# Optimization experiments

Measured on AMD Instinct MI355X. Metric: run time of the kernel, lower is better.

## Reference

```python
import jax, jax.numpy as jnp
import numpy as np


def _procrustes_align(X, Y):
    """Batched similarity-transform (scipy-style Procrustes, reflection allowed).
    Aligns Y (pred) to X (target). X, Y: [B, N, 3]. Returns aligned Y: [B, N, 3].
    """
    muX = X.mean(axis=1, keepdims=True)                      # [B,1,3]
    muY = Y.mean(axis=1, keepdims=True)
    X0 = X - muX
    Y0 = Y - muY
    normX = jnp.sqrt((X0 ** 2).sum(axis=(1, 2), keepdims=True))  # [B,1,1]
    normY = jnp.sqrt((Y0 ** 2).sum(axis=(1, 2), keepdims=True))
    X0n = X0 / normX
    Y0n = Y0 / normY
    # 3x3 cross-covariance per batch element
    M = jnp.einsum('bni,bnj->bij', X0n, Y0n)                 # [B,3,3]
    U, s, Vt = jnp.linalg.svd(M)                             # batched tiny SVD
    # Optimal rotation Q = V @ U^T = (U @ Vt)^T  (minimizes ||Y0n @ Q - X0n||)
    Q = jnp.swapaxes(jnp.matmul(U, Vt), -1, -2)              # [B,3,3]
    traceTA = s.sum(-1)[:, None, None]                       # [B,1,1]
    Z = normX * traceTA * jnp.einsum('bni,bij->bnj', Y0n, Q) + muX
    return Z


def setup_inputs() -> dict:
    key = jax.random.key(0)
    k1, k2 = jax.random.split(key)
    B, N = 262144, 21
    pred_kp3d = jax.random.normal(k1, (B, N, 3), dtype=jnp.float32)
    target_kp3d = jax.random.normal(k2, (B, N, 3), dtype=jnp.float32)
    return {"pred_kp3d": pred_kp3d, "target_kp3d": target_kp3d}


def reference(pred_kp3d, target_kp3d):
    pred_aligned = _procrustes_align(target_kp3d, pred_kp3d)
    # mean per-joint Euclidean distance (PA-MPJPE style)
    err = jnp.sqrt(((pred_aligned - target_kp3d) ** 2).sum(-1)).mean()
    return err
```

## Files before the change

### kernel.cpp

```cpp
#include <hip/hip_runtime.h>
#include <math.h>

#define NPTS 21
#define FLB  63
#define BPB  128
#define THREADS 128
#define NVEC (BPB * FLB / 4)
#define FULL_ROUNDS (NVEC / THREADS)
#define TAIL_LANES  (NVEC % THREADS)

__device__ __forceinline__ void async_cp16(const float* g, float* l) {
    __builtin_amdgcn_global_load_lds(
        (__attribute__((address_space(1))) void*)g,
        (__attribute__((address_space(3))) void*)l,
        16, 0, 0);
}

__global__ __launch_bounds__(THREADS)
void pa_mpjpe(const float* __restrict__ pred,
              const float* __restrict__ targ,
              float* __restrict__ ws,
              int B)
{
    __shared__ __align__(16) float sbuf[BPB * FLB];
    __shared__ float swsum[THREADS / 64];

    const int tid  = threadIdx.x;
    const int lane_u = tid & ~63;
    const int b0   = blockIdx.x * BPB;

    {
        const float* gp = pred + (size_t)b0 * FLB;
        #pragma unroll
        for (int j = 0; j < FULL_ROUNDS; ++j)
            async_cp16(gp + 4 * (j * THREADS + tid), sbuf + 4 * (j * THREADS + lane_u));
        if (tid < TAIL_LANES)
            async_cp16(gp + 4 * (FULL_ROUNDS * THREADS + tid),
                       sbuf + 4 * (FULL_ROUNDS * THREADS + lane_u));
    }
    __builtin_amdgcn_s_waitcnt(0x0F70);
    __syncthreads();

    float y[NPTS][3];
    float sy0 = 0.f, sy1 = 0.f, sy2 = 0.f, syy = 0.f;
    const int base = tid * FLB;
    #pragma unroll
    for (int n = 0; n < NPTS; ++n) {
        float a = sbuf[base + 3*n + 0];
        float b = sbuf[base + 3*n + 1];
        float c = sbuf[base + 3*n + 2];
        y[n][0] = a; y[n][1] = b; y[n][2] = c;
        sy0 += a; sy1 += b; sy2 += c;
        syy = fmaf(a, a, fmaf(b, b, fmaf(c, c, syy)));
    }
    __syncthreads();

    {
        const float* gt = targ + (size_t)b0 * FLB;
        #pragma unroll
        for (int j = 0; j < FULL_ROUNDS; ++j)
            async_cp16(gt + 4 * (j * THREADS + tid), sbuf + 4 * (j * THREADS + lane_u));
        if (tid < TAIL_LANES)
            async_cp16(gt + 4 * (FULL_ROUNDS * THREADS + tid),
                       sbuf + 4 * (FULL_ROUNDS * THREADS + lane_u));
    }
    __builtin_amdgcn_s_waitcnt(0x0F70);
    __syncthreads();

    float sx0 = 0.f, sx1 = 0.f, sx2 = 0.f;
    float m00=0,m01=0,m02=0, m10=0,m11=0,m12=0, m20=0,m21=0,m22=0;
    #pragma unroll
    for (int n = 0; n < NPTS; ++n) {
        float a = sbuf[base + 3*n + 0];
        float b = sbuf[base + 3*n + 1];
        float c = sbuf[base + 3*n + 2];
        sx0 += a; sx1 += b; sx2 += c;
        float u = y[n][0], v = y[n][1], w = y[n][2];
        m00 = fmaf(a,u,m00); m01 = fmaf(a,v,m01); m02 = fmaf(a,w,m02);
        m10 = fmaf(b,u,m10); m11 = fmaf(b,v,m11); m12 = fmaf(b,w,m12);
        m20 = fmaf(c,u,m20); m21 = fmaf(c,v,m21); m22 = fmaf(c,w,m22);
    }

    const float invN = 1.0f / (float)NPTS;
    float mux0 = sx0*invN, mux1 = sx1*invN, mux2 = sx2*invN;
    float muy0 = sy0*invN, muy1 = sy1*invN, muy2 = sy2*invN;
    float ny2  = syy - (sy0*sy0 + sy1*sy1 + sy2*sy2) * invN;
    float c00 = m00 - sx0*sy0*invN, c01 = m01 - sx0*sy1*invN, c02 = m02 - sx0*sy2*invN;
    float c10 = m10 - sx1*sy0*invN, c11 = m11 - sx1*sy1*invN, c12 = m12 - sx1*sy2*invN;
    float c20 = m20 - sx2*sy0*invN, c21 = m21 - sx2*sy1*invN, c22 = m22 - sx2*sy2*invN;

    float q00=c00, q01=c10, q02=c20,
          q10=c01, q11=c11, q12=c21,
          q20=c02, q21=c12, q22=c22;
    #pragma unroll
    for (int it = 0; it < 8; ++it) {
        float C00 = q11*q22 - q12*q21;
        float C01 = q12*q20 - q10*q22;
        float C02 = q10*q21 - q11*q20;
        float C10 = q02*q21 - q01*q22;
        float C11 = q00*q22 - q02*q20;
        float C12 = q01*q20 - q00*q21;
        float C20 = q01*q12 - q02*q11;
        float C21 = q02*q10 - q00*q12;
        float C22 = q00*q11 - q01*q10;
        float det = q00*C00 + q01*C01 + q02*C02;
        float ad  = fmaxf(fabsf(det), 1e-30f);
        float sdet = copysignf(ad, det);
        float g  = __expf(0.333333333f * __logf(ad));
        float ha = 0.5f / g;
        float hb = 0.5f * g / sdet;
        q00 = ha*q00 + hb*C00; q01 = ha*q01 + hb*C01; q02 = ha*q02 + hb*C02;
        q10 = ha*q10 + hb*C10; q11 = ha*q11 + hb*C11; q12 = ha*q12 + hb*C12;
        q20 = ha*q20 + hb*C20; q21 = ha*q21 + hb*C21; q22 = ha*q22 + hb*C22;
    }

    float trP = q00*c00 + q01*c10 + q02*c20
              + q10*c01 + q11*c11 + q12*c21
              + q20*c02 + q21*c12 + q22*c22;
    float k = trP / ny2;
    float r00=k*q00, r01=k*q01, r02=k*q02;
    float r10=k*q10, r11=k*q11, r12=k*q12;
    float r20=k*q20, r21=k*q21, r22=k*q22;

    float errsum = 0.0f;
    #pragma unroll
    for (int n = 0; n < NPTS; ++n) {
        float xa = sbuf[base + 3*n + 0];
        float xb = sbuf[base + 3*n + 1];
        float xc = sbuf[base + 3*n + 2];
        float u = y[n][0] - muy0, v = y[n][1] - muy1, w = y[n][2] - muy2;
        float z0 = fmaf(u, r00, fmaf(v, r10, fmaf(w, r20, mux0))) - xa;
        float z1 = fmaf(u, r01, fmaf(v, r11, fmaf(w, r21, mux1))) - xb;
        float z2 = fmaf(u, r02, fmaf(v, r12, fmaf(w, r22, mux2))) - xc;
        errsum += sqrtf(fmaf(z0, z0, fmaf(z1, z1, z2*z2)));
    }

    #pragma unroll
    for (int off = 32; off > 0; off >>= 1) errsum += __shfl_down(errsum, off, 64);
    if ((tid & 63) == 0) swsum[tid >> 6] = errsum;
    __syncthreads();
    if (tid == 0) ws[blockIdx.x] = swsum[0] + swsum[1];
}

__global__ __launch_bounds__(256)
void pa_reduce(const float* __restrict__ ws, float* __restrict__ out,
               int nblk, float inv_total)
{
    __shared__ float sw[4];
    float s = 0.0f;
    for (int i = threadIdx.x; i < nblk; i += 256) s += ws[i];
    #pragma unroll
    for (int off = 32; off > 0; off >>= 1) s += __shfl_down(s, off, 64);
    if ((threadIdx.x & 63) == 0) sw[threadIdx.x >> 6] = s;
    __syncthreads();
    if (threadIdx.x == 0)
        out[0] = (sw[0] + sw[1] + sw[2] + sw[3]) * inv_total;
}

extern "C" void kernel_launch(void* const* d_in, const int* in_sizes, int n_in,
                              void* d_out, int out_size, void* d_ws, size_t ws_size,
                              hipStream_t stream)
{
    const float* pred = (const float*)d_in[0];
    const float* targ = (const float*)d_in[1];
    float* out = (float*)d_out;
    float* ws  = (float*)d_ws;

    int B = in_sizes[0] / FLB;
    int grid = (B + BPB - 1) / BPB;
    float inv_total = 1.0f / ((float)B * (float)NPTS);

    pa_mpjpe<<<grid, THREADS, 0, stream>>>(pred, targ, ws, B);
    pa_reduce<<<1, 256, 0, stream>>>(ws, out, grid, inv_total);
}
```

Baseline: 149.8 us.

## Split each batch element across four lanes with shuffle reductions, smaller blocks

```diff
diff --git a/kernel.cpp b/kernel.cpp
--- a/kernel.cpp
+++ b/kernel.cpp
@@ -3,11 +3,11 @@
 
 #define NPTS 21
 #define FLB  63
-#define BPB  128
-#define THREADS 128
-#define NVEC (BPB * FLB / 4)
-#define FULL_ROUNDS (NVEC / THREADS)
-#define TAIL_LANES  (NVEC % THREADS)
+#define BPB  16
+#define THREADS 64
+#define TVEC (BPB * FLB / 4)
+#define FULLR (TVEC / THREADS)
+#define TAILL (TVEC % THREADS)
 
 __device__ __forceinline__ void async_cp16(const float* g, float* l) {
     __builtin_amdgcn_global_load_lds(
@@ -16,70 +16,67 @@
         16, 0, 0);
 }
 
-__global__ __launch_bounds__(THREADS)
+__global__ __launch_bounds__(THREADS, 5)
 void pa_mpjpe(const float* __restrict__ pred,
               const float* __restrict__ targ,
               float* __restrict__ ws,
               int B)
 {
-    __shared__ __align__(16) float sbuf[BPB * FLB];
-    __shared__ float swsum[THREADS / 64];
+    __shared__ __align__(16) float ly[BPB * FLB];
+    __shared__ __align__(16) float lx[BPB * FLB];
 
-    const int tid  = threadIdx.x;
-    const int lane_u = tid & ~63;
-    const int b0   = blockIdx.x * BPB;
+    const int tid = threadIdx.x;
+    const int b   = tid & (BPB - 1);
+    const int sub = tid >> 4;
+    const int b0  = blockIdx.x * BPB;
 
     {
         const float* gp = pred + (size_t)b0 * FLB;
+        const float* gt = targ + (size_t)b0 * FLB;
         #pragma unroll
-        for (int j = 0; j < FULL_ROUNDS; ++j)
-            async_cp16(gp + 4 * (j * THREADS + tid), sbuf + 4 * (j * THREADS + lane_u));
-        if (tid < TAIL_LANES)
-            async_cp16(gp + 4 * (FULL_ROUNDS * THREADS + tid),
-                       sbuf + 4 * (FULL_ROUNDS * THREADS + lane_u));
+        for (int j = 0; j < FULLR; ++j)
+            async_cp16(gp + 4 * (j * THREADS + tid), ly + 4 * (j * THREADS));
+        if (tid < TAILL)
+            async_cp16(gp + 4 * (FULLR * THREADS + tid), ly + 4 * (FULLR * THREADS));
+        #pragma unroll
+        for (int j = 0; j < FULLR; ++j)
+            async_cp16(gt + 4 * (j * THREADS + tid), lx + 4 * (j * THREADS));
+        if (tid < TAILL)
+            async_cp16(gt + 4 * (FULLR * THREADS + tid), lx + 4 * (FULLR * THREADS));
     }
     __builtin_amdgcn_s_waitcnt(0x0F70);
-    __syncthreads();
 
-    float y[NPTS][3];
-    float sy0 = 0.f, sy1 = 0.f, sy2 = 0.f, syy = 0.f;
-    const int base = tid * FLB;
+    float py0[6], py1[6], py2[6];
+    float sy0=0.f, sy1=0.f, sy2=0.f, syy=0.f;
+    float sx0=0.f, sx1=0.f, sx2=0.f;
+    float m00=0,m01=0,m02=0, m10=0,m11=0,m12=0, m20=0,m21=0,m22=0;
+    const int base = b * FLB;
     #pragma unroll
-    for (int n = 0; n < NPTS; ++n) {
-        float a = sbuf[base + 3*n + 0];
-        float b = sbuf[base + 3*n + 1];
-        float c = sbuf[base + 3*n + 2];
-        y[n][0] = a; y[n][1] = b; y[n][2] = c;
-        sy0 += a; sy1 += b; sy2 += c;
-        syy = fmaf(a, a, fmaf(b, b, fmaf(c, c, syy)));
+    for (int k = 0; k < 6; ++k) {
+        const int n = sub + 4 * k;
+        if (n < NPTS) {
+            const int o = base + 3 * n;
+            float a = ly[o+0], e = ly[o+1], c = ly[o+2];
+            float u = lx[o+0], v = lx[o+1], w = lx[o+2];
+            py0[k] = a; py1[k] = e; py2[k] = c;
+            sy0 += a; sy1 += e; sy2 += c;
+            syy = fmaf(a, a, fmaf(e, e, fmaf(c, c, syy)));
+            sx0 += u; sx1 += v; sx2 += w;
+            m00 = fmaf(u,a,m00); m01 = fmaf(u,e,m01); m02 = fmaf(u,c,m02);
+            m10 = fmaf(v,a,m10); m11 = fmaf(v,e,m11); m12 = fmaf(v,c,m12);
+            m20 = fmaf(w,a,m20); m21 = fmaf(w,e,m21); m22 = fmaf(w,c,m22);
+        } else {
+            py0[k] = 0.f; py1[k] = 0.f; py2[k] = 0.f;
+        }
     }
-    __syncthreads();
 
-    {
-        const float* gt = targ + (size_t)b0 * FLB;
-        #pragma unroll
-        for (int j = 0; j < FULL_ROUNDS; ++j)
-            async_cp16(gt + 4 * (j * THREADS + tid), sbuf + 4 * (j * THREADS + lane_u));
-        if (tid < TAIL_LANES)
-            async_cp16(gt + 4 * (FULL_ROUNDS * THREADS + tid),
-                       sbuf + 4 * (FULL_ROUNDS * THREADS + lane_u));
-    }
-    __builtin_amdgcn_s_waitcnt(0x0F70);
-    __syncthreads();
-
-    float sx0 = 0.f, sx1 = 0.f, sx2 = 0.f;
-    float m00=0,m01=0,m02=0, m10=0,m11=0,m12=0, m20=0,m21=0,m22=0;
-    #pragma unroll
-    for (int n = 0; n < NPTS; ++n) {
-        float a = sbuf[base + 3*n + 0];
-        float b = sbuf[base + 3*n + 1];
-        float c = sbuf[base + 3*n + 2];
-        sx0 += a; sx1 += b; sx2 += c;
-        float u = y[n][0], v = y[n][1], w = y[n][2];
-        m00 = fmaf(a,u,m00); m01 = fmaf(a,v,m01); m02 = fmaf(a,w,m02);
-        m10 = fmaf(b,u,m10); m11 = fmaf(b,v,m11); m12 = fmaf(b,w,m12);
-        m20 = fmaf(c,u,m20); m21 = fmaf(c,v,m21); m22 = fmaf(c,w,m22);
-    }
+    #define COMB(v) { v += __shfl_xor(v, 16, 64); v += __shfl_xor(v, 32, 64); }
+    COMB(sy0) COMB(sy1) COMB(sy2) COMB(syy)
+    COMB(sx0) COMB(sx1) COMB(sx2)
+    COMB(m00) COMB(m01) COMB(m02)
+    COMB(m10) COMB(m11) COMB(m12)
+    COMB(m20) COMB(m21) COMB(m22)
+    #undef COMB
 
     const float invN = 1.0f / (float)NPTS;
     float mux0 = sx0*invN, mux1 = sx1*invN, mux2 = sx2*invN;
@@ -117,29 +114,29 @@
     float trP = q00*c00 + q01*c10 + q02*c20
               + q10*c01 + q11*c11 + q12*c21
               + q20*c02 + q21*c12 + q22*c22;
-    float k = trP / ny2;
-    float r00=k*q00, r01=k*q01, r02=k*q02;
-    float r10=k*q10, r11=k*q11, r12=k*q12;
-    float r20=k*q20, r21=k*q21, r22=k*q22;
+    float kk = trP / ny2;
+    float r00=kk*q00, r01=kk*q01, r02=kk*q02;
+    float r10=kk*q10, r11=kk*q11, r12=kk*q12;
+    float r20=kk*q20, r21=kk*q21, r22=kk*q22;
 
     float errsum = 0.0f;
     #pragma unroll
-    for (int n = 0; n < NPTS; ++n) {
-        float xa = sbuf[base + 3*n + 0];
-        float xb = sbuf[base + 3*n + 1];
-        float xc = sbuf[base + 3*n + 2];
-        float u = y[n][0] - muy0, v = y[n][1] - muy1, w = y[n][2] - muy2;
-        float z0 = fmaf(u, r00, fmaf(v, r10, fmaf(w, r20, mux0))) - xa;
-        float z1 = fmaf(u, r01, fmaf(v, r11, fmaf(w, r21, mux1))) - xb;
-        float z2 = fmaf(u, r02, fmaf(v, r12, fmaf(w, r22, mux2))) - xc;
-        errsum += sqrtf(fmaf(z0, z0, fmaf(z1, z1, z2*z2)));
+    for (int k = 0; k < 6; ++k) {
+        const int n = sub + 4 * k;
+        if (n < NPTS) {
+            const int o = base + 3 * n;
+            float xa = lx[o+0], xb = lx[o+1], xc = lx[o+2];
+            float u = py0[k] - muy0, v = py1[k] - muy1, w = py2[k] - muy2;
+            float z0 = fmaf(u, r00, fmaf(v, r10, fmaf(w, r20, mux0))) - xa;
+            float z1 = fmaf(u, r01, fmaf(v, r11, fmaf(w, r21, mux1))) - xb;
+            float z2 = fmaf(u, r02, fmaf(v, r12, fmaf(w, r22, mux2))) - xc;
+            errsum += sqrtf(fmaf(z0, z0, fmaf(z1, z1, z2*z2)));
+        }
     }
 
     #pragma unroll
     for (int off = 32; off > 0; off >>= 1) errsum += __shfl_down(errsum, off, 64);
-    if ((tid & 63) == 0) swsum[tid >> 6] = errsum;
-    __syncthreads();
-    if (tid == 0) ws[blockIdx.x] = swsum[0] + swsum[1];
+    if (tid == 0) ws[blockIdx.x] = errsum;
 }
 
 __global__ __launch_bounds__(256)
@@ -148,7 +145,12 @@
 {
     __shared__ float sw[4];
     float s = 0.0f;
-    for (int i = threadIdx.x; i < nblk; i += 256) s += ws[i];
+    const float4* w4 = (const float4*)ws;
+    const int n4 = nblk >> 2;
+    for (int i = threadIdx.x; i < n4; i += 256) {
+        float4 v = w4[i];
+        s += (v.x + v.y) + (v.z + v.w);
+    }
     #pragma unroll
     for (int off = 32; off > 0; off >>= 1) s += __shfl_down(s, off, 64);
     if ((threadIdx.x & 63) == 0) sw[threadIdx.x >> 6] = s;
```

New measurement: 149.8 us. About the same (-0.0%).
